# Optimization experiments

Measured on AMD Instinct MI355X. Metric: run time of the kernel, lower is better.

## Reference

```python
import jax, jax.numpy as jnp
import numpy as np

B, S, H = 2, 2048, 2048
NUM_HEADS, HEAD_DIM, GROUP_SIZE = 16, 128, 4
NUM_KV_HEADS = NUM_HEADS // GROUP_SIZE
ROPE_THETA = 10000.0


def setup_inputs() -> dict:
    key = jax.random.key(0)
    ks = jax.random.split(key, 10)
    xavier = lambda k, fi, fo: jax.random.uniform(k, (fi, fo), jnp.float32,
                                                  -jnp.sqrt(6.0 / (fi + fo)), jnp.sqrt(6.0 / (fi + fo)))
    hidden_states = jax.random.normal(ks[0], (B, S, H), jnp.float32)
    # causal mask: 1.0 where attention is disallowed (strictly upper triangle)
    mask = jnp.triu(jnp.ones((S, S), jnp.float32), k=1)[None, None, :, :]
    mask = jnp.broadcast_to(mask, (B, 1, S, S))
    return {
        "hidden_states": hidden_states,
        "mask": mask,
        "Wq": xavier(ks[1], H, NUM_HEADS * HEAD_DIM), "bq": jnp.zeros((NUM_HEADS * HEAD_DIM,), jnp.float32),
        "Wk": xavier(ks[2], H, NUM_KV_HEADS * HEAD_DIM), "bk": jnp.zeros((NUM_KV_HEADS * HEAD_DIM,), jnp.float32),
        "Wv": xavier(ks[3], H, NUM_KV_HEADS * HEAD_DIM), "bv": jnp.zeros((NUM_KV_HEADS * HEAD_DIM,), jnp.float32),
        "Wo": xavier(ks[4], NUM_HEADS * HEAD_DIM, H), "bo": jnp.zeros((H,), jnp.float32),
    }


def _apply_rope(q, k):
    # q: [b, s, hq, d], k: [b, s, hk, d]
    s, d = q.shape[1], q.shape[-1]
    inv_freq = 1.0 / (ROPE_THETA ** (jnp.arange(0, d, 2, dtype=jnp.float32) / d))  # [d/2]
    angles = jnp.arange(s, dtype=jnp.float32)[:, None] * inv_freq[None, :]          # [s, d/2]
    cos = jnp.cos(angles)[None, :, None, :]  # [1, s, 1, d/2]
    sin = jnp.sin(angles)[None, :, None, :]

    def rot(x):
        x1, x2 = jnp.split(x, 2, axis=-1)
        return jnp.concatenate([x1 * cos - x2 * sin, x1 * sin + x2 * cos], axis=-1)

    return rot(q), rot(k)


def reference(hidden_states, mask, Wq, bq, Wk, bk, Wv, bv, Wo, bo):
    b, s, _ = hidden_states.shape
    scale = 1.0 / jnp.sqrt(jnp.float32(HEAD_DIM))

    q = (hidden_states @ Wq + bq).reshape(b, s, NUM_HEADS, HEAD_DIM)
    k = (hidden_states @ Wk + bk).reshape(b, s, NUM_KV_HEADS, HEAD_DIM)
    v = (hidden_states @ Wv + bv).reshape(b, s, NUM_KV_HEADS, HEAD_DIM)

    q, k = _apply_rope(q, k)

    q = jnp.transpose(q, (0, 2, 1, 3))  # [b, hq, s, d]
    k = jnp.transpose(k, (0, 2, 1, 3))  # [b, hk, s, d]
    v = jnp.transpose(v, (0, 2, 1, 3))

    new_past_key, new_past_value = k, v

    # GQA: repeat each KV head group_size times
    k_rep = jnp.repeat(k, GROUP_SIZE, axis=1)  # [b, hq, s, d]
    v_rep = jnp.repeat(v, GROUP_SIZE, axis=1)

    attn_scores = jnp.einsum('bhqd,bhkd->bhqk', q, k_rep) * scale  # [b, hq, s, s]
    attn_scores = attn_scores + mask * -1e9
    attn_probs = jax.nn.softmax(attn_scores, axis=-1)
    attn_output = jnp.einsum('bhqk,bhkd->bhqd', attn_probs, v_rep)

    attn_output = attn_output.transpose(0, 2, 1, 3).reshape(b, s, NUM_HEADS * HEAD_DIM)
    attn_output = attn_output @ Wo + bo
    return attn_output, new_past_key, new_past_value
```

## Files before the change

### kernel.cpp

```cpp
#include <hip/hip_runtime.h>
#include <stdint.h>

#define S_LEN 2048
#define HDIM  2048
#define N_HEADS 16
#define HEAD_D 128
#define N_KV 4

typedef unsigned short u16;
typedef __attribute__((ext_vector_type(8))) short bf16x8;
typedef __attribute__((ext_vector_type(4))) short bf16x4;
typedef __attribute__((ext_vector_type(4))) float f32x4;

#define MFMA_PV(a, b, c) __builtin_amdgcn_mfma_f32_16x16x16bf16_1k(a, b, c, 0, 0, 0)

__device__ __forceinline__ u16 f2bf(float f) {
  unsigned u = __float_as_uint(f);
  u += 0x7FFFu + ((u >> 16) & 1u);
  return (u16)(u >> 16);
}

__device__ __forceinline__ float bf2f(u16 v) {
  return __uint_as_float(((unsigned)v) << 16);
}

__device__ __forceinline__ void gll16(void* lds, const void* gp) {
  __builtin_amdgcn_global_load_lds(
      (const __attribute__((address_space(1))) void*)gp,
      (__attribute__((address_space(3))) void*)lds, 16, 0, 0);
}

__global__ __launch_bounds__(256) void k_convert(const float* __restrict__ src,
                                                 u16* __restrict__ dst, int n4) {
  int i = blockIdx.x * 256 + threadIdx.x;
  if (i < n4) {
    float4 v = ((const float4*)src)[i];
    ushort4 o;
    o.x = f2bf(v.x); o.y = f2bf(v.y); o.z = f2bf(v.z); o.w = f2bf(v.w);
    ((ushort4*)dst)[i] = o;
  }
}

__global__ __launch_bounds__(256) void k_trig(float2* __restrict__ tab) {
  const float c1 = -13.287712379549449f / 64.f;
  int idx = blockIdx.x * 256 + threadIdx.x;
  int s = idx >> 6, d1 = idx & 63;
  float fr = exp2f((float)d1 * c1);
  float sn, cs;
  sincosf((float)s * fr, &sn, &cs);
  tab[idx] = make_float2(cs, sn);
}

__global__ __launch_bounds__(256) void k_transpose_w(const float* __restrict__ W,
                                                     u16* __restrict__ Wt,
                                                     int K, int N, int perm) {
  __shared__ float tile[64][65];
  int k0 = blockIdx.x * 64, n0 = blockIdx.y * 64;
  int tr = threadIdx.x >> 6, tc = threadIdx.x & 63;
#pragma unroll
  for (int i = 0; i < 16; ++i) {
    int r = tr + i * 4;
    tile[r][tc] = W[(size_t)(k0 + r) * N + n0 + tc];
  }
  __syncthreads();
#pragma unroll
  for (int i = 0; i < 16; ++i) {
    int r = tr + i * 4;
    int nn = n0 + r;
    if (perm)
      nn = (nn & ~127) | ((nn & 15) | ((nn & 48) << 1) | ((nn & 64) >> 2));
    Wt[(size_t)nn * K + k0 + tc] = f2bf(tile[tc][r]);
  }
}

__device__ __forceinline__ void gemm_main_128(
    const u16* __restrict__ A, const u16* __restrict__ Bt,
    int m0, int n0, int K, f32x4 (&acc)[4][4]) {
  __shared__ __align__(16) u16 sA[128 * 32];
  __shared__ __align__(16) u16 sB[128 * 32];
  const int tid = threadIdx.x;
  const int lane = tid & 63;
  const int wave = tid >> 6;
  const int quad = lane >> 4;
  const int l15 = lane & 15;
  const int wm = (wave >> 1) << 6;
  const int wn = (wave & 1) << 6;

#pragma unroll
  for (int i = 0; i < 4; ++i)
#pragma unroll
    for (int j = 0; j < 4; ++j)
      acc[i][j] = (f32x4){0.f, 0.f, 0.f, 0.f};

  for (int kk = 0; kk < K; kk += 32) {
    __syncthreads();
#pragma unroll
    for (int it = 0; it < 2; ++it) {
      int c = tid + (it << 8);
      int row = c >> 2;
      int ko = (c & 3) << 3;
      gll16((char*)sA + c * 16, A + (size_t)(m0 + row) * K + kk + ko);
      gll16((char*)sB + c * 16, Bt + (size_t)(n0 + row) * K + kk + ko);
    }
    __syncthreads();
    bf16x8 af[4], bfr[4];
#pragma unroll
    for (int i = 0; i < 4; ++i)
      af[i] = *(const bf16x8*)&sA[(wm + (i << 4) + l15) * 32 + quad * 8];
#pragma unroll
    for (int j = 0; j < 4; ++j)
      bfr[j] = *(const bf16x8*)&sB[(wn + (j << 4) + l15) * 32 + quad * 8];
#pragma unroll
    for (int i = 0; i < 4; ++i)
#pragma unroll
      for (int j = 0; j < 4; ++j)
        acc[i][j] = __builtin_amdgcn_mfma_f32_16x16x32_bf16(af[i], bfr[j], acc[i][j], 0, 0, 0);
  }
}

__device__ __forceinline__ void gemm_tile_128(
    const u16* __restrict__ A, const u16* __restrict__ Bt,
    const float* __restrict__ bias, float* __restrict__ C,
    int m0, int n0, int K, int ldc) {
  const int tid = threadIdx.x;
  const int lane = tid & 63;
  const int wave = tid >> 6;
  const int quad = lane >> 4;
  const int l15 = lane & 15;
  const int wm = (wave >> 1) << 6;
  const int wn = (wave & 1) << 6;

  f32x4 acc[4][4];
  gemm_main_128(A, Bt, m0, n0, K, acc);

#pragma unroll
  for (int i = 0; i < 4; ++i) {
    int row = m0 + wm + (i << 4) + quad * 4;
#pragma unroll
    for (int j = 0; j < 4; ++j) {
      int col = n0 + wn + (j << 4) + l15;
      float bv = bias[col];
      float* cp = C + (size_t)row * ldc + col;
#pragma unroll
      for (int r = 0; r < 4; ++r)
        cp[(size_t)r * ldc] = acc[i][j][r] + bv;
    }
  }
}

__global__ __launch_bounds__(256) void k_gemm_qkv_fused(
    const u16* __restrict__ X, const u16* __restrict__ Wqt,
    const u16* __restrict__ Wkt, const u16* __restrict__ Wvt,
    const float* __restrict__ bq, const float* __restrict__ bk,
    const float* __restrict__ bv, u16* __restrict__ Qbf,
    u16* __restrict__ Kbf, float* __restrict__ outK,
    float* __restrict__ Vf, const float2* __restrict__ trig) {
  const int m0 = blockIdx.x << 7;
  const int by = blockIdx.y;
  const int tid = threadIdx.x;
  const int lane = tid & 63;
  const int wave = tid >> 6;
  const int quad = lane >> 4;
  const int l15 = lane & 15;
  const int wm = (wave >> 1) << 6;
  const int wn = (wave & 1) << 6;

  const u16* Bt; int n0;
  if (by < 16)      { Bt = Wqt; n0 = by << 7; }
  else if (by < 20) { Bt = Wkt; n0 = (by - 16) << 7; }
  else              { Bt = Wvt; n0 = (by - 20) << 7; }

  f32x4 acc[4][4];
  gemm_main_128(X, Bt, m0, n0, 2048, acc);

  if (by < 16) {
    const float qscale = 0.08838834764831845f * 1.4426950408889634f;
    const int h = by;
#pragma unroll
    for (int jp = 0; jp < 2; ++jp) {
      const int d1 = (((wn >> 5) + jp) << 4) + l15;
      const float b1 = bq[h * 128 + d1];
      const float b2 = bq[h * 128 + d1 + 64];
#pragma unroll
      for (int i = 0; i < 4; ++i) {
        const int rowb = m0 + wm + (i << 4) + quad * 4;
#pragma unroll
        for (int r = 0; r < 4; ++r) {
          const int tok = rowb + r;
          const int b = tok >> 11, s = tok & 2047;
          const float2 t = trig[(s << 6) + d1];
          float x1 = acc[i][2 * jp][r] + b1;
          float x2 = acc[i][2 * jp + 1][r] + b2;
          u16* dst = Qbf + ((size_t)(b * N_HEADS + h) * S_LEN + s) * HEAD_D + d1;
          dst[0]  = f2bf((x1 * t.x - x2 * t.y) * qscale);
          dst[64] = f2bf((x1 * t.y + x2 * t.x) * qscale);
        }
      }
    }
  } else if (by < 20) {
    const int kvh = by - 16;
#pragma unroll
    for (int jp = 0; jp < 2; ++jp) {
      const int d1 = (((wn >> 5) + jp) << 4) + l15;
      const float b1 = bk[kvh * 128 + d1];
      const float b2 = bk[kvh * 128 + d1 + 64];
#pragma unroll
      for (int i = 0; i < 4; ++i) {
        const int rowb = m0 + wm + (i << 4) + quad * 4;
#pragma unroll
        for (int r = 0; r < 4; ++r) {
          const int tok = rowb + r;
          const int b = tok >> 11, s = tok & 2047;
          const float2 t = trig[(s << 6) + d1];
          float x1 = acc[i][2 * jp][r] + b1;
          float x2 = acc[i][2 * jp + 1][r] + b2;
          float o1 = x1 * t.x - x2 * t.y;
          float o2 = x1 * t.y + x2 * t.x;
          size_t idx = ((size_t)(b * N_KV + kvh) * S_LEN + s) * HEAD_D + d1;
          Kbf[idx]      = f2bf(o1);
          Kbf[idx + 64] = f2bf(o2);
          outK[idx]      = o1;
          outK[idx + 64] = o2;
        }
      }
    }
  } else {
#pragma unroll
    for (int i = 0; i < 4; ++i) {
      int row = m0 + wm + (i << 4) + quad * 4;
#pragma unroll
      for (int j = 0; j < 4; ++j) {
        int col = n0 + wn + (j << 4) + l15;
        float bvv = bv[col];
        float* cp = Vf + (size_t)row * 512 + col;
#pragma unroll
        for (int r = 0; r < 4; ++r)
          cp[(size_t)r * 512] = acc[i][j][r] + bvv;
      }
    }
  }
}

__global__ __launch_bounds__(256) void k_gemm_o(
    const u16* __restrict__ A, const u16* __restrict__ Wot,
    const float* __restrict__ bo, float* __restrict__ C) {
  gemm_tile_128(A, Wot, bo, C, blockIdx.x << 7, blockIdx.y << 7, 2048, 2048);
}

__global__ __launch_bounds__(256) void k_vtrans(const float* __restrict__ Vf,
                                                u16* __restrict__ Vt,
                                                float* __restrict__ outV) {
  __shared__ float tile[64][65];
  int s0 = blockIdx.x * 64, d0 = blockIdx.y * 64;
  int z = blockIdx.z;
  int b = z >> 2, kvh = z & 3;
  int tr = threadIdx.x >> 6, tc = threadIdx.x & 63;
#pragma unroll
  for (int i = 0; i < 16; ++i) {
    int r = tr + i * 4;
    float v = Vf[(size_t)(b * S_LEN + s0 + r) * 512 + kvh * 128 + d0 + tc];
    tile[r][tc] = v;
    outV[((size_t)z * S_LEN + s0 + r) * HEAD_D + d0 + tc] = v;
  }
  __syncthreads();
#pragma unroll
  for (int i = 0; i < 16; ++i) {
    int r = tr + i * 4;
    Vt[((size_t)z * HEAD_D + d0 + r) * S_LEN + s0 + tc] = f2bf(tile[tc][r]);
  }
}

__global__ __launch_bounds__(256, 2) void k_attn(
    const u16* __restrict__ Qbf, const u16* __restrict__ Kbf,
    const u16* __restrict__ Vt, u16* __restrict__ attn,
    u16* __restrict__ pO, float* __restrict__ pML) {
  __shared__ __align__(16) u16 smem[17920];
  u16* sK = smem;
  u16* sV = smem + 8704;

  const int tid = threadIdx.x;
  const int lane = tid & 63;
  const int wave = tid >> 6;
  const int quad = lane >> 4;
  const int l15 = lane & 15;

  const int by = blockIdx.y;
  int qt, t0, t1, slot;
  bool finalw;
  if (by < 8) {
    qt = 8 + by; t0 = 0; t1 = 16; finalw = false;
    slot = ((blockIdx.x << 3) + (qt - 8)) << 1;
  } else {
    qt = 23 - by;
    if (qt >= 8) {
      t0 = 16; t1 = 2 * qt + 2; finalw = false;
      slot = (((blockIdx.x << 3) + (qt - 8)) << 1) + 1;
    } else {
      t0 = 0; t1 = 2 * qt + 2; finalw = true; slot = 0;
    }
  }

  const int bh = blockIdx.x;
  const int b = bh >> 4;
  const int h = bh & 15;
  const int kvh = h >> 2;
  const int q0 = qt << 7;
  const int qw = q0 + wave * 32;

  const u16* Qb = Qbf + ((size_t)(b * N_HEADS + h) * S_LEN + qw) * HEAD_D;
  const u16* Kb = Kbf + (size_t)(b * N_KV + kvh) * S_LEN * HEAD_D;
  const u16* Vb = Vt + (size_t)(b * N_KV + kvh) * HEAD_D * S_LEN;

  bf16x8 aq[2][4];
#pragma unroll
  for (int i = 0; i < 2; ++i)
#pragma unroll
    for (int kc = 0; kc < 4; ++kc)
      aq[i][kc] = *(const bf16x8*)(Qb + (size_t)(i * 16 + l15) * HEAD_D + kc * 32 + quad * 8);

  float mst[2] = {-1e30f, -1e30f}, lst[2] = {0.f, 0.f};
  f32x4 oacc[2][8];
#pragma unroll
  for (int i = 0; i < 2; ++i)
#pragma unroll
    for (int n = 0; n < 8; ++n) oacc[i][n] = (f32x4){0.f, 0.f, 0.f, 0.f};

  for (int t = t0; t < t1; ++t) {
    const int kt0 = t << 6;
    __syncthreads();
#pragma unroll
    for (int it = 0; it < 9; ++it) {
      int c = tid + (it << 8);
      if (c < 1088) {
        int row = c / 17;
        int k16 = c - row * 17;
        gll16((char*)sK + c * 16, Kb + (size_t)(kt0 + row) * HEAD_D + k16 * 8);
      } else if (c < 2240) {
        int vv = c - 1088;
        int d = vv / 9;
        int s16 = vv - d * 9;
        gll16((char*)sV + vv * 16, Vb + (size_t)d * S_LEN + kt0 + s16 * 8);
      }
    }
    __syncthreads();

    if (kt0 > qw + 31) continue;

    f32x4 st[2][4];
#pragma unroll
    for (int i = 0; i < 2; ++i)
#pragma unroll
      for (int j = 0; j < 4; ++j) st[i][j] = (f32x4){0.f, 0.f, 0.f, 0.f};
#pragma unroll
    for (int kc = 0; kc < 4; ++kc) {
#pragma unroll
      for (int j = 0; j < 4; ++j) {
        bf16x8 kf = *(const bf16x8*)&sK[(j * 16 + l15) * 136 + kc * 32 + quad * 8];
#pragma unroll
        for (int i = 0; i < 2; ++i)
          st[i][j] = __builtin_amdgcn_mfma_f32_16x16x32_bf16(kf, aq[i][kc], st[i][j], 0, 0, 0);
      }
    }

    if (kt0 + 63 > qw) {
#pragma unroll
      for (int i = 0; i < 2; ++i) {
        int q = qw + i * 16 + l15;
#pragma unroll
        for (int j = 0; j < 4; ++j) {
          int s = kt0 + j * 16 + quad * 4;
#pragma unroll
          for (int r = 0; r < 4; ++r)
            if (s + r > q) st[i][j][r] = -1e9f;
        }
      }
    }

    bf16x4 pf[2][4];
    float al[2];
#pragma unroll
    for (int i = 0; i < 2; ++i) {
      float m = -1e30f;
#pragma unroll
      for (int j = 0; j < 4; ++j)
#pragma unroll
        for (int r = 0; r < 4; ++r) m = fmaxf(m, st[i][j][r]);
      m = fmaxf(m, __shfl_xor(m, 16, 64));
      m = fmaxf(m, __shfl_xor(m, 32, 64));
      float mn = fmaxf(mst[i], m);
      al[i] = exp2f(mst[i] - mn);
      mst[i] = mn;
      float rs = 0.f;
#pragma unroll
      for (int j = 0; j < 4; ++j) {
        float p0 = exp2f(st[i][j][0] - mn);
        float p1 = exp2f(st[i][j][1] - mn);
        float p2 = exp2f(st[i][j][2] - mn);
        float p3 = exp2f(st[i][j][3] - mn);
        rs += (p0 + p1) + (p2 + p3);
        union { unsigned u[2]; bf16x4 v; } pk;
        pk.u[0] = __builtin_amdgcn_perm(__float_as_uint(p1) + 0x8000u,
                                        __float_as_uint(p0) + 0x8000u, 0x07060302u);
        pk.u[1] = __builtin_amdgcn_perm(__float_as_uint(p3) + 0x8000u,
                                        __float_as_uint(p2) + 0x8000u, 0x07060302u);
        pf[i][j] = pk.v;
      }
      rs += __shfl_xor(rs, 16, 64);
      rs += __shfl_xor(rs, 32, 64);
      lst[i] = lst[i] * al[i] + rs;
#pragma unroll
      for (int r = 0; r < 4; ++r) {
        float a = __shfl(al[i], quad * 4 + r, 16);
#pragma unroll
        for (int n = 0; n < 8; ++n) oacc[i][n][r] *= a;
      }
    }

#pragma unroll
    for (int j = 0; j < 4; ++j) {
#pragma unroll
      for (int n = 0; n < 8; ++n) {
        bf16x4 vf = *(const bf16x4*)&sV[(n * 16 + l15) * 72 + j * 16 + quad * 4];
#pragma unroll
        for (int i = 0; i < 2; ++i)
          oacc[i][n] = MFMA_PV(pf[i][j], vf, oacc[i][n]);
      }
    }
  }

  if (finalw) {
#pragma unroll
    for (int i = 0; i < 2; ++i)
#pragma unroll
      for (int r = 0; r < 4; ++r) {
        float inv = 1.0f / __shfl(lst[i], quad * 4 + r, 16);
        int row = qw + i * 16 + quad * 4 + r;
        u16* op = attn + ((size_t)b * S_LEN + row) * HDIM + h * HEAD_D;
#pragma unroll
        for (int n = 0; n < 8; ++n)
          op[n * 16 + l15] = f2bf(oacc[i][n][r] * inv);
      }
  } else {
    u16* po = pO + (size_t)slot * 16384;
#pragma unroll
    for (int i = 0; i < 2; ++i)
#pragma unroll
      for (int r = 0; r < 4; ++r) {
        int row = wave * 32 + i * 16 + quad * 4 + r;
#pragma unroll
        for (int n = 0; n < 8; ++n)
          po[row * 128 + n * 16 + l15] = f2bf(oacc[i][n][r]);
      }
    if (quad == 0) {
      float* ml = pML + slot * 256;
#pragma unroll
      for (int i = 0; i < 2; ++i) {
        int row = wave * 32 + i * 16 + l15;
        ml[row] = mst[i];
        ml[128 + row] = lst[i];
      }
    }
  }
}

__global__ __launch_bounds__(256) void k_attn_combine(
    const u16* __restrict__ pO, const float* __restrict__ pML,
    u16* __restrict__ attn) {
  const int bh = blockIdx.x;
  const int qt = 8 + blockIdx.y;
  const int b = bh >> 4;
  const int h = bh & 15;
  const int s0 = ((bh << 3) + blockIdx.y) << 1;
  const int row = threadIdx.x >> 1;
  const int half = threadIdx.x & 1;

  const float* ml0 = pML + s0 * 256;
  const float* ml1 = pML + (s0 + 1) * 256;
  float m0 = ml0[row], l0 = ml0[128 + row];
  float m1 = ml1[row], l1 = ml1[128 + row];
  float m = fmaxf(m0, m1);
  float w0 = exp2f(m0 - m), w1 = exp2f(m1 - m);
  float inv = 1.0f / (l0 * w0 + l1 * w1);
  w0 *= inv; w1 *= inv;

  const u16* o0 = pO + (size_t)s0 * 16384 + row * 128 + half * 64;
  const u16* o1 = o0 + 16384;
  u16* op = attn + ((size_t)(b * S_LEN + (qt << 7) + row)) * HDIM + h * HEAD_D + half * 64;
#pragma unroll
  for (int k = 0; k < 8; ++k) {
    ushort4 a0 = ((const ushort4*)o0)[k * 2];
    ushort4 b0 = ((const ushort4*)o0)[k * 2 + 1];
    ushort4 a1 = ((const ushort4*)o1)[k * 2];
    ushort4 b1 = ((const ushort4*)o1)[k * 2 + 1];
    ushort4 ra, rb;
    ra.x = f2bf(bf2f(a0.x) * w0 + bf2f(a1.x) * w1);
    ra.y = f2bf(bf2f(a0.y) * w0 + bf2f(a1.y) * w1);
    ra.z = f2bf(bf2f(a0.z) * w0 + bf2f(a1.z) * w1);
    ra.w = f2bf(bf2f(a0.w) * w0 + bf2f(a1.w) * w1);
    rb.x = f2bf(bf2f(b0.x) * w0 + bf2f(b1.x) * w1);
    rb.y = f2bf(bf2f(b0.y) * w0 + bf2f(b1.y) * w1);
    rb.z = f2bf(bf2f(b0.z) * w0 + bf2f(b1.z) * w1);
    rb.w = f2bf(bf2f(b0.w) * w0 + bf2f(b1.w) * w1);
    ((ushort4*)op)[k * 2] = ra;
    ((ushort4*)op)[k * 2 + 1] = rb;
  }
}

extern "C" void kernel_launch(void* const* d_in, const int* in_sizes, int n_in,
                              void* d_out, int out_size, void* d_ws, size_t ws_size,
                              hipStream_t stream) {
  (void)in_sizes; (void)n_in; (void)out_size; (void)ws_size;
  const float* hs = (const float*)d_in[0];
  const float* Wq = (const float*)d_in[2];
  const float* bq = (const float*)d_in[3];
  const float* Wk = (const float*)d_in[4];
  const float* bk = (const float*)d_in[5];
  const float* Wv = (const float*)d_in[6];
  const float* bv = (const float*)d_in[7];
  const float* Wo = (const float*)d_in[8];
  const float* bo = (const float*)d_in[9];
  float* out = (float*)d_out;

  char* ws = (char*)d_ws;
  u16* Xbf   = (u16*)(ws + 0);
  u16* Wqt   = (u16*)(ws + 16777216);
  u16* Wkt   = (u16*)(ws + 25165824);
  u16* Wvt   = (u16*)(ws + 27262976);
  u16* Wot   = (u16*)(ws + 29360128);
  float* Vf  = (float*)(ws + 79691776);
  u16* Qbf   = (u16*)(ws + 88080384);
  u16* Kbf   = (u16*)(ws + 104857600);
  u16* Vtb   = (u16*)(ws + 109051904);
  u16* attnb = (u16*)(ws + 37748736);
  float* pML = (float*)(ws + 54525952);
  float2* trg = (float2*)(ws + 56623104);
  u16* pO    = (u16*)(ws + 71303168);

  k_trig<<<512, 256, 0, stream>>>(trg);
  k_convert<<<8192, 256, 0, stream>>>(hs, Xbf, 2097152);
  k_transpose_w<<<dim3(32, 32), 256, 0, stream>>>(Wq, Wqt, 2048, 2048, 1);
  k_transpose_w<<<dim3(32, 8), 256, 0, stream>>>(Wk, Wkt, 2048, 512, 1);
  k_transpose_w<<<dim3(32, 8), 256, 0, stream>>>(Wv, Wvt, 2048, 512, 0);
  k_transpose_w<<<dim3(32, 32), 256, 0, stream>>>(Wo, Wot, 2048, 2048, 0);
  k_gemm_qkv_fused<<<dim3(32, 24), 256, 0, stream>>>(
      Xbf, Wqt, Wkt, Wvt, bq, bk, bv, Qbf, Kbf, out + 8388608, Vf, trg);
  k_vtrans<<<dim3(32, 2, 8), 256, 0, stream>>>(Vf, Vtb, out + 10485760);
  k_attn<<<dim3(32, 24), 256, 0, stream>>>(Qbf, Kbf, Vtb, attnb, pO, pML);
  k_attn_combine<<<dim3(32, 8), 256, 0, stream>>>(pO, pML, attnb);
  k_gemm_o<<<dim3(32, 16), 256, 0, stream>>>(attnb, Wot, bo, out);
}
```

Baseline: 378.7 us.

## Merge prep kernels into one launch and fuse V transpose into QKV epilogue

Six small preprocessing launches (trig table, input conversion, four weight transposes) are combined into a single kernel that dispatches on block index. The separate V transpose kernel is removed: the QKV GEMM epilogue now writes the fp32 V output and the transposed bf16 V directly, which eliminates the fp32 V intermediate buffer and its round trip through memory. The cost is that the epilogue's transposed bf16 stores are 8-byte writes spread across rows, so they coalesce less well than the old tiled transpose.

```diff
diff --git a/kernel.cpp b/kernel.cpp
--- a/kernel.cpp
+++ b/kernel.cpp
@@ -30,32 +30,10 @@
       (__attribute__((address_space(3))) void*)lds, 16, 0, 0);
 }
 
-__global__ __launch_bounds__(256) void k_convert(const float* __restrict__ src,
-                                                 u16* __restrict__ dst, int n4) {
-  int i = blockIdx.x * 256 + threadIdx.x;
-  if (i < n4) {
-    float4 v = ((const float4*)src)[i];
-    ushort4 o;
-    o.x = f2bf(v.x); o.y = f2bf(v.y); o.z = f2bf(v.z); o.w = f2bf(v.w);
-    ((ushort4*)dst)[i] = o;
-  }
-}
-
-__global__ __launch_bounds__(256) void k_trig(float2* __restrict__ tab) {
-  const float c1 = -13.287712379549449f / 64.f;
-  int idx = blockIdx.x * 256 + threadIdx.x;
-  int s = idx >> 6, d1 = idx & 63;
-  float fr = exp2f((float)d1 * c1);
-  float sn, cs;
-  sincosf((float)s * fr, &sn, &cs);
-  tab[idx] = make_float2(cs, sn);
-}
-
-__global__ __launch_bounds__(256) void k_transpose_w(const float* __restrict__ W,
-                                                     u16* __restrict__ Wt,
-                                                     int K, int N, int perm) {
-  __shared__ float tile[64][65];
-  int k0 = blockIdx.x * 64, n0 = blockIdx.y * 64;
+__device__ __forceinline__ void wtrans_body(
+    const float* __restrict__ W, u16* __restrict__ Wt, int K, int N,
+    int perm, int flat, float (*tile)[65]) {
+  int k0 = (flat & 31) * 64, n0 = (flat >> 5) * 64;
   int tr = threadIdx.x >> 6, tc = threadIdx.x & 63;
 #pragma unroll
   for (int i = 0; i < 16; ++i) {
@@ -70,6 +48,40 @@
     if (perm)
       nn = (nn & ~127) | ((nn & 15) | ((nn & 48) << 1) | ((nn & 64) >> 2));
     Wt[(size_t)nn * K + k0 + tc] = f2bf(tile[tc][r]);
+  }
+}
+
+__global__ __launch_bounds__(256) void k_prep(
+    const float* __restrict__ hs, u16* __restrict__ Xbf,
+    const float* __restrict__ Wq, u16* __restrict__ Wqt,
+    const float* __restrict__ Wk, u16* __restrict__ Wkt,
+    const float* __restrict__ Wv, u16* __restrict__ Wvt,
+    const float* __restrict__ Wo, u16* __restrict__ Wot,
+    float2* __restrict__ trig) {
+  __shared__ float tile[64][65];
+  const int bid = blockIdx.x;
+  if (bid < 8192) {
+    int i = bid * 256 + threadIdx.x;
+    float4 v = ((const float4*)hs)[i];
+    ushort4 o;
+    o.x = f2bf(v.x); o.y = f2bf(v.y); o.z = f2bf(v.z); o.w = f2bf(v.w);
+    ((ushort4*)Xbf)[i] = o;
+  } else if (bid < 9216) {
+    wtrans_body(Wq, Wqt, 2048, 2048, 1, bid - 8192, tile);
+  } else if (bid < 9472) {
+    wtrans_body(Wk, Wkt, 2048, 512, 1, bid - 9216, tile);
+  } else if (bid < 9728) {
+    wtrans_body(Wv, Wvt, 2048, 512, 0, bid - 9472, tile);
+  } else if (bid < 10752) {
+    wtrans_body(Wo, Wot, 2048, 2048, 0, bid - 9728, tile);
+  } else {
+    const float c1 = -13.287712379549449f / 64.f;
+    int idx = (bid - 10752) * 256 + threadIdx.x;
+    int s = idx >> 6, d1 = idx & 63;
+    float fr = exp2f((float)d1 * c1);
+    float sn, cs;
+    sincosf((float)s * fr, &sn, &cs);
+    trig[idx] = make_float2(cs, sn);
   }
 }
 
@@ -154,7 +166,8 @@
     const float* __restrict__ bq, const float* __restrict__ bk,
     const float* __restrict__ bv, u16* __restrict__ Qbf,
     u16* __restrict__ Kbf, float* __restrict__ outK,
-    float* __restrict__ Vf, const float2* __restrict__ trig) {
+    u16* __restrict__ Vt, float* __restrict__ outV,
+    const float2* __restrict__ trig) {
   const int m0 = blockIdx.x << 7;
   const int by = blockIdx.y;
   const int tid = threadIdx.x;
@@ -225,17 +238,28 @@
       }
     }
   } else {
+    const int kvh = by - 20;
 #pragma unroll
     for (int i = 0; i < 4; ++i) {
-      int row = m0 + wm + (i << 4) + quad * 4;
+      const int rowb = m0 + wm + (i << 4) + quad * 4;
+      const int b = rowb >> 11, s = rowb & 2047;
+      const int z = b * N_KV + kvh;
 #pragma unroll
       for (int j = 0; j < 4; ++j) {
-        int col = n0 + wn + (j << 4) + l15;
-        float bvv = bv[col];
-        float* cp = Vf + (size_t)row * 512 + col;
-#pragma unroll
-        for (int r = 0; r < 4; ++r)
-          cp[(size_t)r * 512] = acc[i][j][r] + bvv;
+        const int d = wn + (j << 4) + l15;
+        const float bvv = bv[kvh * 128 + d];
+        float v0 = acc[i][j][0] + bvv;
+        float v1 = acc[i][j][1] + bvv;
+        float v2 = acc[i][j][2] + bvv;
+        float v3 = acc[i][j][3] + bvv;
+        float* ov = outV + ((size_t)z * S_LEN + s) * HEAD_D + d;
+        ov[0]   = v0;
+        ov[128] = v1;
+        ov[256] = v2;
+        ov[384] = v3;
+        ushort4 pk;
+        pk.x = f2bf(v0); pk.y = f2bf(v1); pk.z = f2bf(v2); pk.w = f2bf(v3);
+        *(ushort4*)(Vt + ((size_t)z * HEAD_D + d) * S_LEN + s) = pk;
       }
     }
   }
@@ -245,29 +269,6 @@
     const u16* __restrict__ A, const u16* __restrict__ Wot,
     const float* __restrict__ bo, float* __restrict__ C) {
   gemm_tile_128(A, Wot, bo, C, blockIdx.x << 7, blockIdx.y << 7, 2048, 2048);
-}
-
-__global__ __launch_bounds__(256) void k_vtrans(const float* __restrict__ Vf,
-                                                u16* __restrict__ Vt,
-                                                float* __restrict__ outV) {
-  __shared__ float tile[64][65];
-  int s0 = blockIdx.x * 64, d0 = blockIdx.y * 64;
-  int z = blockIdx.z;
-  int b = z >> 2, kvh = z & 3;
-  int tr = threadIdx.x >> 6, tc = threadIdx.x & 63;
-#pragma unroll
-  for (int i = 0; i < 16; ++i) {
-    int r = tr + i * 4;
-    float v = Vf[(size_t)(b * S_LEN + s0 + r) * 512 + kvh * 128 + d0 + tc];
-    tile[r][tc] = v;
-    outV[((size_t)z * S_LEN + s0 + r) * HEAD_D + d0 + tc] = v;
-  }
-  __syncthreads();
-#pragma unroll
-  for (int i = 0; i < 16; ++i) {
-    int r = tr + i * 4;
-    Vt[((size_t)z * HEAD_D + d0 + r) * S_LEN + s0 + tc] = f2bf(tile[tc][r]);
-  }
 }
 
 __global__ __launch_bounds__(256, 2) void k_attn(
@@ -527,7 +528,6 @@
   u16* Wkt   = (u16*)(ws + 25165824);
   u16* Wvt   = (u16*)(ws + 27262976);
   u16* Wot   = (u16*)(ws + 29360128);
-  float* Vf  = (float*)(ws + 79691776);
   u16* Qbf   = (u16*)(ws + 88080384);
   u16* Kbf   = (u16*)(ws + 104857600);
   u16* Vtb   = (u16*)(ws + 109051904);
@@ -536,15 +536,10 @@
   float2* trg = (float2*)(ws + 56623104);
   u16* pO    = (u16*)(ws + 71303168);
 
-  k_trig<<<512, 256, 0, stream>>>(trg);
-  k_convert<<<8192, 256, 0, stream>>>(hs, Xbf, 2097152);
-  k_transpose_w<<<dim3(32, 32), 256, 0, stream>>>(Wq, Wqt, 2048, 2048, 1);
-  k_transpose_w<<<dim3(32, 8), 256, 0, stream>>>(Wk, Wkt, 2048, 512, 1);
-  k_transpose_w<<<dim3(32, 8), 256, 0, stream>>>(Wv, Wvt, 2048, 512, 0);
-  k_transpose_w<<<dim3(32, 32), 256, 0, stream>>>(Wo, Wot, 2048, 2048, 0);
+  k_prep<<<11264, 256, 0, stream>>>(hs, Xbf, Wq, Wqt, Wk, Wkt, Wv, Wvt, Wo, Wot, trg);
   k_gemm_qkv_fused<<<dim3(32, 24), 256, 0, stream>>>(
-      Xbf, Wqt, Wkt, Wvt, bq, bk, bv, Qbf, Kbf, out + 8388608, Vf, trg);
-  k_vtrans<<<dim3(32, 2, 8), 256, 0, stream>>>(Vf, Vtb, out + 10485760);
+      Xbf, Wqt, Wkt, Wvt, bq, bk, bv, Qbf, Kbf, out + 8388608,
+      Vtb, out + 10485760, trg);
   k_attn<<<dim3(32, 24), 256, 0, stream>>>(Qbf, Kbf, Vtb, attnb, pO, pML);
   k_attn_combine<<<dim3(32, 8), 256, 0, stream>>>(pO, pML, attnb);
   k_gemm_o<<<dim3(32, 16), 256, 0, stream>>>(attnb, Wot, bo, out);
```

Measured after the change: 365.4 us. -3.5%, faster.
